# Kernel tuning notes

Hardware: AMD Instinct MI355X
Metric: run time of the kernel (lower is better)

Reference implementation:

```python
import jax, jax.numpy as jnp
import numpy as np

D = 1024      # n_embd
NH = 16       # attention heads
E = 8         # n_experts
K = 2         # k_best
FF = 4 * D    # expert MLP hidden
EPS = 1e-6    # rms_norm_epsilon
TEMP = 1.0    # target_temperature


def setup_inputs() -> dict:
    key = jax.random.key(0)
    ks = jax.random.split(key, 12)
    B, S = 2, 1024
    s = 0.02
    return {
        "x": jax.random.normal(ks[0], (B, S, D), jnp.float32),
        "attn_norm_w": jnp.ones((D,), jnp.float32),
        "wq": jax.random.normal(ks[1], (D, D), jnp.float32) * s,
        "wk": jax.random.normal(ks[2], (D, D), jnp.float32) * s,
        "wv": jax.random.normal(ks[3], (D, D), jnp.float32) * s,
        "wo": jax.random.normal(ks[4], (D, D), jnp.float32) * s,
        "mlp_norm_w": jnp.ones((D,), jnp.float32),
        "router_w": jax.random.normal(ks[5], (D, E), jnp.float32) * s,
        "w1": jax.random.normal(ks[6], (E, D, FF), jnp.float32) * s,
        "b1": jnp.zeros((E, FF), jnp.float32),
        "w2": jax.random.normal(ks[7], (E, FF, D), jnp.float32) * s,
        "b2": jnp.zeros((E, D), jnp.float32),
    }


def _rmsnorm(x, w):
    var = jnp.mean(jnp.square(x), axis=-1, keepdims=True)
    return x * jax.lax.rsqrt(var + EPS) * w


def _attention(x, wq, wk, wv, wo):
    B, S, _ = x.shape
    dh = D // NH
    q = (x @ wq).reshape(B, S, NH, dh)
    k = (x @ wk).reshape(B, S, NH, dh)
    v = (x @ wv).reshape(B, S, NH, dh)
    scores = jnp.einsum("bqhd,bkhd->bhqk", q, k) / jnp.sqrt(jnp.float32(dh))
    causal = jnp.tril(jnp.ones((S, S), bool))  # [S,S]
    scores = jnp.where(causal[None, None], scores, jnp.finfo(scores.dtype).min)
    attn = jax.nn.softmax(scores, axis=-1)
    out = jnp.einsum("bhqk,bkhd->bqhd", attn, v).reshape(B, S, D)
    return out @ wo


def reference(x, attn_norm_w, wq, wk, wv, wo, mlp_norm_w, router_w, w1, b1, w2, b2):
    B, S, _ = x.shape
    # attention sub-block
    x = x + _attention(_rmsnorm(x, attn_norm_w), wq, wk, wv, wo)
    residual = x
    h = _rmsnorm(x, mlp_norm_w)  # [B,S,D]

    # router: temperature softmax + top-k
    logits = h @ router_w / TEMP                      # [B,S,E]
    probs = jax.nn.softmax(logits, axis=-1)
    top_k_scores, top_k_indices = jax.lax.top_k(probs, K)  # [B,S,K]
    onehot = jax.nn.one_hot(top_k_indices, E, dtype=h.dtype)  # [B,S,K,E]
    gates = jnp.einsum("bsk,bske->bse", top_k_scores, onehot)  # [B,S,E]

    # load-balancing loss (Switch-style) + expert counts
    counts = jnp.sum(onehot, axis=(0, 1, 2))          # [E]
    frac = counts / (B * S * K)
    mean_prob = jnp.mean(probs, axis=(0, 1))          # [E]
    balancing_loss = E * jnp.sum(frac * mean_prob)

    # experts: dense dispatch; tokens with zero gate contribute nothing,
    # so this matches the sort/gather/scatter top-k combine exactly.
    pre = jnp.einsum("bsd,edf->ebsf", h, w1) + b1[:, None, None]  # [E,B,S,FF]
    act = jax.nn.gelu(pre)
    y = jnp.einsum("ebsf,efd->ebsd", act, w2) + b2[:, None, None]  # [E,B,S,D]
    moe = jnp.einsum("ebsd,bse->bsd", y, gates)

    out = residual + moe
    return out, balancing_loss, counts
```

## Files before the change

### kernel.cpp

```cpp
#include <hip/hip_runtime.h>

typedef __bf16 bf16;
typedef __bf16 bf16x4 __attribute__((ext_vector_type(4)));
typedef __bf16 bf16x8 __attribute__((ext_vector_type(8)));
typedef float f32x4 __attribute__((ext_vector_type(4)));

#define D_   1024
#define S_   1024
#define B_   2
#define NTOK 2048
#define FF_  4096
#define NE   8
#define CAP  5120
#define OUTN 2097152

__device__ __forceinline__ float gelu_f(float x) {
    float u = 0.7978845608028654f * (x + 0.044715f * x * x * x);
    float a = fabsf(u);
    float e = __expf(-2.0f * a);
    float t = (1.0f - e) / (1.0f + e);
    t = copysignf(t, u);
    return 0.5f * x * (1.0f + t);
}

__device__ __forceinline__ void gload16(const void* g, void* l) {
    __builtin_amdgcn_global_load_lds((const __attribute__((address_space(1))) unsigned int*)g,
                                     (__attribute__((address_space(3))) unsigned int*)l,
                                     16, 0, 0);
}

#define VMCNT(n) asm volatile("s_waitcnt vmcnt(" n ")" ::: "memory")
#define BARRIER() do { asm volatile("" ::: "memory"); \
                       __builtin_amdgcn_s_barrier();  \
                       asm volatile("" ::: "memory"); } while (0)

__global__ __launch_bounds__(256) void rmsnorm_k(const float* __restrict__ x,
                                                 const float* __restrict__ w,
                                                 float* __restrict__ yf,
                                                 bf16* __restrict__ yhi,
                                                 bf16* __restrict__ ylo) {
    int row = blockIdx.x;
    int t = threadIdx.x;
    const float* xr = x + (size_t)row * D_;
    float4 v = *(const float4*)(xr + t * 4);
    float ss = v.x * v.x + v.y * v.y + v.z * v.z + v.w * v.w;
    for (int off = 32; off; off >>= 1) ss += __shfl_down(ss, off);
    __shared__ float wsum[4];
    if ((t & 63) == 0) wsum[t >> 6] = ss;
    __syncthreads();
    float tot = wsum[0] + wsum[1] + wsum[2] + wsum[3];
    float rr = rsqrtf(tot * (1.0f / D_) + 1e-6f);
    float4 wv = *(const float4*)(w + t * 4);
    float y[4];
    y[0] = v.x * rr * wv.x; y[1] = v.y * rr * wv.y;
    y[2] = v.z * rr * wv.z; y[3] = v.w * rr * wv.w;
    if (yf) *(float4*)(yf + (size_t)row * D_ + t * 4) = *(float4*)y;
    if (yhi) {
#pragma unroll
        for (int i = 0; i < 4; i++) {
            bf16 hi = (bf16)y[i];
            yhi[(size_t)row * D_ + t * 4 + i] = hi;
            if (ylo) ylo[(size_t)row * D_ + t * 4 + i] = (bf16)(y[i] - (float)hi);
        }
    }
}

__global__ __launch_bounds__(256) void trans_split_k(
    const float* __restrict__ w0, const float* __restrict__ w1p,
    const float* __restrict__ w2p, const float* __restrict__ w3,
    bf16* o0h, bf16* o0l, bf16* o1h, bf16* o1l,
    bf16* o2h, bf16* o2l, bf16* o3h, bf16* o3l) {
    int z = blockIdx.z;
    const float* src = (z == 0) ? w0 : (z == 1) ? w1p : (z == 2) ? w2p : w3;
    bf16* dh = (z == 0) ? o0h : (z == 1) ? o1h : (z == 2) ? o2h : o3h;
    bf16* dl = (z == 0) ? o0l : (z == 1) ? o1l : (z == 2) ? o2l : o3l;
    __shared__ float tl[32][33];
    int c0 = blockIdx.x * 32, r0 = blockIdx.y * 32;
    int tx = threadIdx.x & 31, ty = threadIdx.x >> 5;
#pragma unroll
    for (int i = 0; i < 4; i++) {
        int r = ty + i * 8;
        tl[r][tx] = src[(size_t)(r0 + r) * 1024 + c0 + tx];
    }
    __syncthreads();
#pragma unroll
    for (int i = 0; i < 4; i++) {
        int c = ty + i * 8;
        float v = tl[tx][c];
        bf16 hi = (bf16)v;
        dh[(size_t)(c0 + c) * 1024 + r0 + tx] = hi;
        dl[(size_t)(c0 + c) * 1024 + r0 + tx] = (bf16)(v - (float)hi);
    }
}

__global__ __launch_bounds__(256) void transpose_cast4_k(const float* __restrict__ in,
                                                         bf16* __restrict__ out,
                                                         int R, int C) {
    __shared__ float tl[64][65];
    size_t base = (size_t)blockIdx.z * R * C;
    const float* src = in + base;
    bf16* dst = out + base;
    int c0 = blockIdx.x * 64, r0 = blockIdx.y * 64;
    int t = threadIdx.x;
    int lr = t >> 4;
    int lc = (t & 15) * 4;
#pragma unroll
    for (int i = 0; i < 4; i++) {
        int r = lr + i * 16;
        float4 v = *(const float4*)(src + (size_t)(r0 + r) * C + c0 + lc);
        tl[r][lc] = v.x; tl[r][lc + 1] = v.y; tl[r][lc + 2] = v.z; tl[r][lc + 3] = v.w;
    }
    __syncthreads();
    int wc = t >> 4;
    int wr = (t & 15) * 4;
#pragma unroll
    for (int i = 0; i < 4; i++) {
        int c = wc + i * 16;
        bf16x4 o;
        o[0] = (bf16)tl[wr][c];     o[1] = (bf16)tl[wr + 1][c];
        o[2] = (bf16)tl[wr + 2][c]; o[3] = (bf16)tl[wr + 3][c];
        *(bf16x4*)(dst + (size_t)(c0 + c) * R + r0 + wr) = o;
    }
}

#define SPLIT_STAGE(bi, k0)                             \
    gload16(gah0 + (k0), Lah[bi] + wv * 512);           \
    gload16(gah1 + (k0), Lah[bi] + 2048 + wv * 512);    \
    gload16(gal0 + (k0), Lal[bi] + wv * 512);           \
    gload16(gal1 + (k0), Lal[bi] + 2048 + wv * 512);    \
    gload16(gbh0 + (k0), Lbh[bi] + wv * 512);           \
    gload16(gbh1 + (k0), Lbh[bi] + 2048 + wv * 512);    \
    gload16(gbl0 + (k0), Lbl[bi] + wv * 512);           \
    gload16(gbl1 + (k0), Lbl[bi] + 2048 + wv * 512);

#define SPLIT_COMPUTE(bi) {                                                            \
    bf16x8 fah[4], fal[4], fbh[4], fbl[4];                                             \
    _Pragma("unroll") for (int i = 0; i < 4; i++) {                                    \
        fah[i] = *(const bf16x8*)(Lah[bi] + ra_off[i]);                                \
        fal[i] = *(const bf16x8*)(Lal[bi] + ra_off[i]);                                \
        fbh[i] = *(const bf16x8*)(Lbh[bi] + rb_off[i]);                                \
        fbl[i] = *(const bf16x8*)(Lbl[bi] + rb_off[i]);                                \
    }                                                                                  \
    _Pragma("unroll") for (int mt = 0; mt < 4; mt++)                                   \
    _Pragma("unroll") for (int nt = 0; nt < 4; nt++) {                                 \
        acc[mt][nt] = __builtin_amdgcn_mfma_f32_16x16x32_bf16(fah[mt], fbh[nt], acc[mt][nt], 0, 0, 0); \
        acc[mt][nt] = __builtin_amdgcn_mfma_f32_16x16x32_bf16(fah[mt], fbl[nt], acc[mt][nt], 0, 0, 0); \
        acc[mt][nt] = __builtin_amdgcn_mfma_f32_16x16x32_bf16(fal[mt], fbh[nt], acc[mt][nt], 0, 0, 0); \
    } }

#define GEMM128_SPLIT_BODY(EPILOGUE)                                                   \
    __shared__ __align__(16) bf16 Lah[2][4096];                                        \
    __shared__ __align__(16) bf16 Lal[2][4096];                                        \
    __shared__ __align__(16) bf16 Lbh[2][4096];                                        \
    __shared__ __align__(16) bf16 Lbl[2][4096];                                        \
    int t = threadIdx.x;                                                               \
    int wv = t >> 6, ln = t & 63;                                                      \
    int wm = wv >> 1, wn = wv & 1, l15 = ln & 15, qd = ln >> 4;                        \
    int sr0 = t >> 2, sr1 = 64 + sr0, cl = t & 3;                                      \
    int cs0 = (cl ^ ((sr0 >> 1) & 3)) * 8;                                             \
    int cs1 = (cl ^ ((sr1 >> 1) & 3)) * 8;                                             \
    const bf16* gah0 = Ah + (size_t)(m0 + sr0) * 1024 + cs0;                           \
    const bf16* gah1 = Ah + (size_t)(m0 + sr1) * 1024 + cs1;                           \
    const bf16* gal0 = Al + (size_t)(m0 + sr0) * 1024 + cs0;                           \
    const bf16* gal1 = Al + (size_t)(m0 + sr1) * 1024 + cs1;                           \
    const bf16* gbh0 = Bh + (size_t)(n0 + sr0) * 1024 + cs0;                           \
    const bf16* gbh1 = Bh + (size_t)(n0 + sr1) * 1024 + cs1;                           \
    const bf16* gbl0 = Bl + (size_t)(n0 + sr0) * 1024 + cs0;                           \
    const bf16* gbl1 = Bl + (size_t)(n0 + sr1) * 1024 + cs1;                           \
    int ra_off[4], rb_off[4];                                                          \
    _Pragma("unroll") for (int i = 0; i < 4; i++) {                                    \
        int r1 = wm * 64 + i * 16 + l15;                                               \
        ra_off[i] = r1 * 32 + (qd ^ ((r1 >> 1) & 3)) * 8;                              \
        int r2 = wn * 64 + i * 16 + l15;                                               \
        rb_off[i] = r2 * 32 + (qd ^ ((r2 >> 1) & 3)) * 8;                              \
    }                                                                                  \
    f32x4 acc[4][4];                                                                   \
    _Pragma("unroll") for (int mt = 0; mt < 4; mt++)                                   \
    _Pragma("unroll") for (int nt = 0; nt < 4; nt++) acc[mt][nt] = (f32x4){0.f,0.f,0.f,0.f}; \
    SPLIT_STAGE(0, 0);                                                                 \
    __syncthreads();                                                                   \
    for (int k0 = 0; k0 < 1024; k0 += 64) {                                            \
        SPLIT_STAGE(1, k0 + 32);                                                       \
        SPLIT_COMPUTE(0);                                                              \
        __syncthreads();                                                               \
        if (k0 + 64 < 1024) { SPLIT_STAGE(0, k0 + 64); }                               \
        SPLIT_COMPUTE(1);                                                              \
        __syncthreads();                                                               \
    }                                                                                  \
    _Pragma("unroll") for (int mt = 0; mt < 4; mt++)                                   \
    _Pragma("unroll") for (int nt = 0; nt < 4; nt++)                                   \
        _Pragma("unroll") for (int r = 0; r < 4; r++) {                                \
            int gm = m0 + wm * 64 + mt * 16 + qd * 4 + r;                              \
            int gn = n0 + wn * 64 + nt * 16 + l15;                                     \
            float vv = acc[mt][nt][r];                                                 \
            EPILOGUE                                                                   \
        }

__global__ __launch_bounds__(256) void gemm_qkv_k(
    const bf16* __restrict__ Ah, const bf16* __restrict__ Al,
    const bf16* __restrict__ Bqh, const bf16* __restrict__ Bql,
    const bf16* __restrict__ Bkh, const bf16* __restrict__ Bkl,
    const bf16* __restrict__ Bvh, const bf16* __restrict__ Bvl,
    bf16* Cqh, bf16* Cql, bf16* Ckh, bf16* Ckl, bf16* Cvh, bf16* Cvl) {
    int gy = blockIdx.y, zw = gy >> 3;
    const bf16* Bh = (zw == 0) ? Bqh : (zw == 1) ? Bkh : Bvh;
    const bf16* Bl = (zw == 0) ? Bql : (zw == 1) ? Bkl : Bvl;
    bf16* Ch = (zw == 0) ? Cqh : (zw == 1) ? Ckh : Cvh;
    bf16* Cl = (zw == 0) ? Cql : (zw == 1) ? Ckl : Cvl;
    int m0 = blockIdx.x * 128, n0 = (gy & 7) * 128;
    GEMM128_SPLIT_BODY({
        bf16 hi = (bf16)vv;
        Ch[(size_t)gm * D_ + gn] = hi;
        Cl[(size_t)gm * D_ + gn] = (bf16)(vv - (float)hi);
    })
}

__global__ __launch_bounds__(256) void gemm_wo_k(
    const bf16* __restrict__ Ah, const bf16* __restrict__ Al,
    const bf16* __restrict__ Bh, const bf16* __restrict__ Bl,
    float* __restrict__ C, const float* __restrict__ X) {
    int m0 = blockIdx.x * 128, n0 = blockIdx.y * 128;
    GEMM128_SPLIT_BODY({
        C[(size_t)gm * D_ + gn] = X[(size_t)gm * D_ + gn] + vv;
    })
}

#define AP 72

__global__ __launch_bounds__(256) void attn_mfma_k(
    const bf16* __restrict__ qhp, const bf16* __restrict__ qlp,
    const bf16* __restrict__ khp, const bf16* __restrict__ klp,
    const bf16* __restrict__ vhp, const bf16* __restrict__ vlp,
    bf16* __restrict__ aoh, bf16* __restrict__ aol) {
    int qt = (int)gridDim.x - 1 - (int)blockIdx.x;
    int h = blockIdx.y, b = blockIdx.z;
    __shared__ bf16 Ksh[64 * AP], Ksl[64 * AP], VTh[64 * AP], VTl[64 * AP];
    __shared__ bf16 Ph[4][16 * AP], Pl[4][16 * AP];
    int t = threadIdx.x, wv = t >> 6, ln = t & 63, l15 = ln & 15, qd = ln >> 4;

    bf16x8 aqh[2], aql[2];
    {
        size_t qb = ((size_t)(b * S_ + qt * 64 + wv * 16 + l15)) * D_ + h * 64 + qd * 8;
        aqh[0] = *(const bf16x8*)(qhp + qb);
        aqh[1] = *(const bf16x8*)(qhp + qb + 32);
        aql[0] = *(const bf16x8*)(qlp + qb);
        aql[1] = *(const bf16x8*)(qlp + qb + 32);
    }
    f32x4 oacc[4];
    float mrow[4], lrow[4];
#pragma unroll
    for (int i = 0; i < 4; i++) {
        oacc[i] = (f32x4){0.f, 0.f, 0.f, 0.f};
        mrow[i] = -1e30f; lrow[i] = 0.0f;
    }

    for (int kt = 0; kt <= qt; kt++) {
        __syncthreads();
#pragma unroll
        for (int j = 0; j < 2; j++) {
            int idx = t + j * 256;
            int row = idx >> 3, ch = (idx & 7) * 8;
            size_t g = ((size_t)(b * S_ + kt * 64 + row)) * D_ + h * 64 + ch;
            *(bf16x8*)&Ksh[row * AP + ch] = *(const bf16x8*)(khp + g);
            *(bf16x8*)&Ksl[row * AP + ch] = *(const bf16x8*)(klp + g);
            bf16x8 vvh = *(const bf16x8*)(vhp + g);
            bf16x8 vvl = *(const bf16x8*)(vlp + g);
#pragma unroll
            for (int jj = 0; jj < 8; jj++) {
                VTh[(ch + jj) * AP + row] = vvh[jj];
                VTl[(ch + jj) * AP + row] = vvl[jj];
            }
        }
        __syncthreads();

        f32x4 sacc[4];
#pragma unroll
        for (int nt = 0; nt < 4; nt++) sacc[nt] = (f32x4){0.f, 0.f, 0.f, 0.f};
#pragma unroll
        for (int ks = 0; ks < 2; ks++) {
#pragma unroll
            for (int nt = 0; nt < 4; nt++) {
                bf16x8 bh = *(const bf16x8*)&Ksh[(nt * 16 + l15) * AP + ks * 32 + qd * 8];
                bf16x8 bl = *(const bf16x8*)&Ksl[(nt * 16 + l15) * AP + ks * 32 + qd * 8];
                sacc[nt] = __builtin_amdgcn_mfma_f32_16x16x32_bf16(aqh[ks], bh, sacc[nt], 0, 0, 0);
                sacc[nt] = __builtin_amdgcn_mfma_f32_16x16x32_bf16(aqh[ks], bl, sacc[nt], 0, 0, 0);
                sacc[nt] = __builtin_amdgcn_mfma_f32_16x16x32_bf16(aql[ks], bh, sacc[nt], 0, 0, 0);
            }
        }
        bool diag = (kt == qt);
#pragma unroll
        for (int r = 0; r < 4; r++) {
            float s0[4];
#pragma unroll
            for (int nt = 0; nt < 4; nt++) {
                s0[nt] = sacc[nt][r] * 0.125f;
                if (diag && (nt * 16 + l15) > (wv * 16 + qd * 4 + r)) s0[nt] = -1e30f;
            }
            float vmax = fmaxf(fmaxf(s0[0], s0[1]), fmaxf(s0[2], s0[3]));
            for (int off = 1; off < 16; off <<= 1) vmax = fmaxf(vmax, __shfl_xor(vmax, off));
            float mnew = fmaxf(mrow[r], vmax);
            float alpha = __expf(mrow[r] - mnew);
            float p[4], rs = 0.0f;
#pragma unroll
            for (int nt = 0; nt < 4; nt++) { p[nt] = __expf(s0[nt] - mnew); rs += p[nt]; }
            for (int off = 1; off < 16; off <<= 1) rs += __shfl_xor(rs, off);
            lrow[r] = lrow[r] * alpha + rs;
            mrow[r] = mnew;
#pragma unroll
            for (int nt = 0; nt < 4; nt++) oacc[nt][r] *= alpha;
            int prow = qd * 4 + r;
#pragma unroll
            for (int nt = 0; nt < 4; nt++) {
                bf16 hi = (bf16)p[nt];
                Ph[wv][prow * AP + nt * 16 + l15] = hi;
                Pl[wv][prow * AP + nt * 16 + l15] = (bf16)(p[nt] - (float)hi);
            }
        }
#pragma unroll
        for (int ks2 = 0; ks2 < 2; ks2++) {
            bf16x8 aph = *(const bf16x8*)&Ph[wv][l15 * AP + ks2 * 32 + qd * 8];
            bf16x8 apl = *(const bf16x8*)&Pl[wv][l15 * AP + ks2 * 32 + qd * 8];
#pragma unroll
            for (int nt = 0; nt < 4; nt++) {
                bf16x8 bvh = *(const bf16x8*)&VTh[(nt * 16 + l15) * AP + ks2 * 32 + qd * 8];
                bf16x8 bvl = *(const bf16x8*)&VTl[(nt * 16 + l15) * AP + ks2 * 32 + qd * 8];
                oacc[nt] = __builtin_amdgcn_mfma_f32_16x16x32_bf16(aph, bvh, oacc[nt], 0, 0, 0);
                oacc[nt] = __builtin_amdgcn_mfma_f32_16x16x32_bf16(aph, bvl, oacc[nt], 0, 0, 0);
                oacc[nt] = __builtin_amdgcn_mfma_f32_16x16x32_bf16(apl, bvh, oacc[nt], 0, 0, 0);
            }
        }
    }

#pragma unroll
    for (int r = 0; r < 4; r++) {
        float inv = 1.0f / lrow[r];
        size_t rowa = ((size_t)(b * S_ + qt * 64 + wv * 16 + qd * 4 + r)) * D_ + h * 64;
#pragma unroll
        for (int nt = 0; nt < 4; nt++) {
            float o = oacc[nt][r] * inv;
            bf16 hi = (bf16)o;
            aoh[rowa + nt * 16 + l15] = hi;
            aol[rowa + nt * 16 + l15] = (bf16)(o - (float)hi);
        }
    }
}

__global__ __launch_bounds__(256) void router_k(const float* __restrict__ h,
                                                const float* __restrict__ rw,
                                                int* __restrict__ tidx,
                                                float* __restrict__ tgate,
                                                int* __restrict__ ecnt,
                                                float* __restrict__ psum) {
    int wv = threadIdx.x >> 6, ln = threadIdx.x & 63;
    int tok = blockIdx.x * 4 + wv;
    const float* hr = h + (size_t)tok * D_;
    float acc[NE];
#pragma unroll
    for (int e = 0; e < NE; e++) acc[e] = 0.0f;
    int base = ln * 16;
#pragma unroll
    for (int c = 0; c < 4; c++) {
        float4 hv = *(const float4*)(hr + base + c * 4);
        const float* rp = rw + (size_t)(base + c * 4) * NE;
        float hx[4] = {hv.x, hv.y, hv.z, hv.w};
#pragma unroll
        for (int jj = 0; jj < 4; jj++)
#pragma unroll
            for (int e = 0; e < NE; e++)
                acc[e] = fmaf(hx[jj], rp[jj * NE + e], acc[e]);
    }
#pragma unroll
    for (int e = 0; e < NE; e++)
        for (int off = 32; off; off >>= 1) acc[e] += __shfl_down(acc[e], off);

    __shared__ float pb[4][NE];
    if (ln == 0) {
        float mx = acc[0];
#pragma unroll
        for (int e = 1; e < NE; e++) mx = fmaxf(mx, acc[e]);
        float p[NE], ssum = 0.0f;
#pragma unroll
        for (int e = 0; e < NE; e++) { p[e] = expf(acc[e] - mx); ssum += p[e]; }
        float inv = 1.0f / ssum;
#pragma unroll
        for (int e = 0; e < NE; e++) p[e] *= inv;
        int i0 = 0; float b0 = p[0];
#pragma unroll
        for (int e = 1; e < NE; e++) if (p[e] > b0) { b0 = p[e]; i0 = e; }
        int i1 = -1; float b1v = -1.0f;
#pragma unroll
        for (int e = 0; e < NE; e++) if (e != i0 && p[e] > b1v) { b1v = p[e]; i1 = e; }
        tidx[tok * 2] = i0; tidx[tok * 2 + 1] = i1;
        tgate[tok * 2] = b0; tgate[tok * 2 + 1] = b1v;
        atomicAdd(&ecnt[i0], 1);
        atomicAdd(&ecnt[i1], 1);
#pragma unroll
        for (int e = 0; e < NE; e++) pb[wv][e] = p[e];
    }
    __syncthreads();
    if (threadIdx.x < NE) {
        float s2 = pb[0][threadIdx.x] + pb[1][threadIdx.x] + pb[2][threadIdx.x] + pb[3][threadIdx.x];
        atomicAdd(&psum[threadIdx.x], s2);
    }
}

__global__ void passb_k(const int* __restrict__ ecnt, const float* __restrict__ psum,
                        int* __restrict__ eoffp, int* __restrict__ ecnt2,
                        float* __restrict__ out_tail) {
    if (threadIdx.x == 0) {
        int off = 0; float loss = 0.0f;
        for (int e = 0; e < NE; e++) {
            eoffp[e] = off;
            int c = ecnt[e];
            off += (c + 127) & ~127;
            loss += (c * (1.0f / 4096.0f)) * (psum[e] * (1.0f / 2048.0f));
            out_tail[1 + e] = (float)c;
            ecnt2[e] = 0;
        }
        eoffp[NE] = off;
        out_tail[0] = 8.0f * loss;
    }
}

__global__ __launch_bounds__(256) void scatter_k(const int* __restrict__ tidx,
                                                 const int* __restrict__ eoffp,
                                                 int* __restrict__ ecnt2,
                                                 int* __restrict__ stok,
                                                 int* __restrict__ sidx) {
    int tok = blockIdx.x * 256 + threadIdx.x;
    for (int k = 0; k < 2; k++) {
        int e = tidx[tok * 2 + k];
        int pos = eoffp[e] + atomicAdd(&ecnt2[e], 1);
        stok[pos] = tok;
        sidx[tok * 2 + k] = pos;
    }
}

#define MOE_STAGE(bufA, bufB, k0)                       \
    gload16(ga0 + (k0), (bufA) + wv * 512);             \
    gload16(ga1 + (k0), (bufA) + 2048 + wv * 512);      \
    gload16(gb0 + (k0), (bufB) + wv * 512);             \
    gload16(gb1 + (k0), (bufB) + 2048 + wv * 512);

#define MOE_TILE(bufA, bufB) {                                                         \
    bf16x8 af[4], bfr[4];                                                              \
    _Pragma("unroll") for (int i = 0; i < 4; i++) {                                    \
        af[i]  = *(const bf16x8*)((bufA) + ra_off[i]);                                 \
        bfr[i] = *(const bf16x8*)((bufB) + rb_off[i]);                                 \
    }                                                                                  \
    _Pragma("unroll") for (int mt = 0; mt < 4; mt++)                                   \
    _Pragma("unroll") for (int nt = 0; nt < 4; nt++)                                   \
        acc[mt][nt] = __builtin_amdgcn_mfma_f32_16x16x32_bf16(af[mt], bfr[nt], acc[mt][nt], 0, 0, 0); }

#define MOE_STEP(rdA, rdB, VM)      \
    VMCNT(VM);                      \
    BARRIER();                      \
    MOE_TILE(rdA, rdB);             \
    BARRIER();

__global__ __launch_bounds__(256) void moe_gemm1_k(const bf16* __restrict__ hB,
                                                   const bf16* __restrict__ w1t,
                                                   const float* __restrict__ b1,
                                                   const int* __restrict__ eoffp,
                                                   const int* __restrict__ stok,
                                                   bf16* __restrict__ act) {
    int m0 = blockIdx.x * 128, n0 = blockIdx.y * 128;
    if (m0 >= eoffp[NE]) return;
    int e = 0;
#pragma unroll
    for (int i = 1; i < NE; i++) if (m0 >= eoffp[i]) e = i;

    __shared__ __align__(16) bf16 As[2][4096];
    __shared__ __align__(16) bf16 Bs[2][4096];
    int t = threadIdx.x;
    int wv = t >> 6, ln = t & 63;
    int wm = wv >> 1, wn = wv & 1, l15 = ln & 15, qd = ln >> 4;

    int sr0 = t >> 2, sr1 = 64 + sr0, cl = t & 3;
    int cs0 = (cl ^ ((sr0 >> 1) & 3)) * 8;
    int cs1 = (cl ^ ((sr1 >> 1) & 3)) * 8;
    const bf16* ga0 = hB + (size_t)stok[m0 + sr0] * D_ + cs0;
    const bf16* ga1 = hB + (size_t)stok[m0 + sr1] * D_ + cs1;
    const bf16* Bb = w1t + ((size_t)e * FF_ + n0) * D_;
    const bf16* gb0 = Bb + (size_t)sr0 * D_ + cs0;
    const bf16* gb1 = Bb + (size_t)sr1 * D_ + cs1;

    int ra_off[4], rb_off[4];
#pragma unroll
    for (int i = 0; i < 4; i++) {
        int r1 = wm * 64 + i * 16 + l15;
        ra_off[i] = r1 * 32 + (qd ^ ((r1 >> 1) & 3)) * 8;
        int r2 = wn * 64 + i * 16 + l15;
        rb_off[i] = r2 * 32 + (qd ^ ((r2 >> 1) & 3)) * 8;
    }

    f32x4 acc[4][4];
#pragma unroll
    for (int mt = 0; mt < 4; mt++)
#pragma unroll
        for (int nt = 0; nt < 4; nt++) acc[mt][nt] = (f32x4){0.f, 0.f, 0.f, 0.f};

    MOE_STAGE(As[0], Bs[0], 0);
    for (int k0 = 0; k0 < 960; k0 += 64) {
        MOE_STAGE(As[1], Bs[1], k0 + 32);
        MOE_STEP(As[0], Bs[0], "4");
        MOE_STAGE(As[0], Bs[0], k0 + 64);
        MOE_STEP(As[1], Bs[1], "4");
    }
    MOE_STAGE(As[1], Bs[1], 992);
    MOE_STEP(As[0], Bs[0], "4");
    MOE_STEP(As[1], Bs[1], "0");

    const float* b1e = b1 + (size_t)e * FF_;
#pragma unroll
    for (int mt = 0; mt < 4; mt++)
#pragma unroll
        for (int nt = 0; nt < 4; nt++) {
            int gn = n0 + wn * 64 + nt * 16 + l15;
            float bias = b1e[gn];
#pragma unroll
            for (int r = 0; r < 4; r++) {
                int gm = m0 + wm * 64 + mt * 16 + qd * 4 + r;
                act[(size_t)gm * FF_ + gn] = (bf16)gelu_f(acc[mt][nt][r] + bias);
            }
        }
}

__global__ __launch_bounds__(256) void moe_gemm2_k(const bf16* __restrict__ act,
                                                   const bf16* __restrict__ w2t,
                                                   const float* __restrict__ b2,
                                                   const int* __restrict__ eoffp,
                                                   float* __restrict__ y) {
    int m0 = blockIdx.x * 128, n0 = blockIdx.y * 128;
    if (m0 >= eoffp[NE]) return;
    int e = 0;
#pragma unroll
    for (int i = 1; i < NE; i++) if (m0 >= eoffp[i]) e = i;
    int zk = blockIdx.z;
    int kbase = zk * 2048;

    __shared__ __align__(16) bf16 As[4][4096];
    __shared__ __align__(16) bf16 Bs[4][4096];
    int t = threadIdx.x;
    int wv = t >> 6, ln = t & 63;
    int wm = wv >> 1, wn = wv & 1, l15 = ln & 15, qd = ln >> 4;

    int sr0 = t >> 2, sr1 = 64 + sr0, cl = t & 3;
    int cs0 = (cl ^ ((sr0 >> 1) & 3)) * 8;
    int cs1 = (cl ^ ((sr1 >> 1) & 3)) * 8;
    const bf16* ga0 = act + (size_t)(m0 + sr0) * FF_ + kbase + cs0;
    const bf16* ga1 = act + (size_t)(m0 + sr1) * FF_ + kbase + cs1;
    const bf16* Bb = w2t + ((size_t)e * D_ + n0) * FF_;
    const bf16* gb0 = Bb + (size_t)sr0 * FF_ + kbase + cs0;
    const bf16* gb1 = Bb + (size_t)sr1 * FF_ + kbase + cs1;

    int ra_off[4], rb_off[4];
#pragma unroll
    for (int i = 0; i < 4; i++) {
        int r1 = wm * 64 + i * 16 + l15;
        ra_off[i] = r1 * 32 + (qd ^ ((r1 >> 1) & 3)) * 8;
        int r2 = wn * 64 + i * 16 + l15;
        rb_off[i] = r2 * 32 + (qd ^ ((r2 >> 1) & 3)) * 8;
    }

    f32x4 acc[4][4];
#pragma unroll
    for (int mt = 0; mt < 4; mt++)
#pragma unroll
        for (int nt = 0; nt < 4; nt++) acc[mt][nt] = (f32x4){0.f, 0.f, 0.f, 0.f};

    MOE_STAGE(As[0], Bs[0], 0);
    MOE_STAGE(As[1], Bs[1], 32);
    for (int k0 = 0; k0 < 1920; k0 += 128) {
        MOE_STAGE(As[2], Bs[2], k0 + 64);  MOE_STEP(As[0], Bs[0], "8");
        MOE_STAGE(As[3], Bs[3], k0 + 96);  MOE_STEP(As[1], Bs[1], "8");
        MOE_STAGE(As[0], Bs[0], k0 + 128); MOE_STEP(As[2], Bs[2], "8");
        MOE_STAGE(As[1], Bs[1], k0 + 160); MOE_STEP(As[3], Bs[3], "8");
    }
    MOE_STAGE(As[2], Bs[2], 1984); MOE_STEP(As[0], Bs[0], "8");
    MOE_STAGE(As[3], Bs[3], 2016); MOE_STEP(As[1], Bs[1], "8");
    MOE_STEP(As[2], Bs[2], "4");
    MOE_STEP(As[3], Bs[3], "0");

    const float* b2e = b2 + (size_t)e * D_;
#pragma unroll
    for (int mt = 0; mt < 4; mt++)
#pragma unroll
        for (int nt = 0; nt < 4; nt++) {
            int gn = n0 + wn * 64 + nt * 16 + l15;
            float bias = (zk == 0) ? b2e[gn] : 0.0f;
#pragma unroll
            for (int r = 0; r < 4; r++) {
                int gm = m0 + wm * 64 + mt * 16 + qd * 4 + r;
                atomicAdd(&y[(size_t)gm * D_ + gn], acc[mt][nt][r] + bias);
            }
        }
}

__global__ __launch_bounds__(256) void combine_k(const float* __restrict__ y,
                                                 const int* __restrict__ sidx,
                                                 const float* __restrict__ tgate,
                                                 float* __restrict__ out) {
    int tok = blockIdx.x;
    int d = threadIdx.x * 4;
    int s0 = sidx[tok * 2], s1 = sidx[tok * 2 + 1];
    float g0 = tgate[tok * 2], g1 = tgate[tok * 2 + 1];
    float4 a = *(const float4*)(y + (size_t)s0 * D_ + d);
    float4 b = *(const float4*)(y + (size_t)s1 * D_ + d);
    float4 o = *(const float4*)(out + (size_t)tok * D_ + d);
    o.x += g0 * a.x + g1 * b.x;
    o.y += g0 * a.y + g1 * b.y;
    o.z += g0 * a.z + g1 * b.z;
    o.w += g0 * a.w + g1 * b.w;
    *(float4*)(out + (size_t)tok * D_ + d) = o;
}

extern "C" void kernel_launch(void* const* d_in, const int* in_sizes, int n_in,
                              void* d_out, int out_size, void* d_ws, size_t ws_size,
                              hipStream_t stream) {
    const float* x   = (const float*)d_in[0];
    const float* anw = (const float*)d_in[1];
    const float* wq  = (const float*)d_in[2];
    const float* wk  = (const float*)d_in[3];
    const float* wv  = (const float*)d_in[4];
    const float* wo  = (const float*)d_in[5];
    const float* mnw = (const float*)d_in[6];
    const float* rw  = (const float*)d_in[7];
    const float* w1  = (const float*)d_in[8];
    const float* b1  = (const float*)d_in[9];
    const float* w2  = (const float*)d_in[10];
    const float* b2  = (const float*)d_in[11];
    float* out = (float*)d_out;

    char* p = (char*)d_ws;
    auto take = [&](size_t n) { char* r = p; p += (n + 255) & ~(size_t)255; return r; };
    bf16* h1h = (bf16*)take((size_t)OUTN * 2);
    bf16* h1l = (bf16*)take((size_t)OUTN * 2);
    bf16* qh  = (bf16*)take((size_t)OUTN * 2);
    bf16* ql  = (bf16*)take((size_t)OUTN * 2);
    bf16* kh  = (bf16*)take((size_t)OUTN * 2);
    bf16* kl  = (bf16*)take((size_t)OUTN * 2);
    bf16* vh  = (bf16*)take((size_t)OUTN * 2);
    bf16* vl  = (bf16*)take((size_t)OUTN * 2);
    bf16* wqth = (bf16*)take((size_t)D_ * D_ * 2);
    bf16* wqtl = (bf16*)take((size_t)D_ * D_ * 2);
    bf16* wkth = (bf16*)take((size_t)D_ * D_ * 2);
    bf16* wktl = (bf16*)take((size_t)D_ * D_ * 2);
    bf16* wvth = (bf16*)take((size_t)D_ * D_ * 2);
    bf16* wvtl = (bf16*)take((size_t)D_ * D_ * 2);
    bf16* woth = (bf16*)take((size_t)D_ * D_ * 2);
    bf16* wotl = (bf16*)take((size_t)D_ * D_ * 2);
    bf16* w1t = (bf16*)take((size_t)NE * FF_ * D_ * 2);
    bf16* w2t = (bf16*)take((size_t)NE * FF_ * D_ * 2);
    bf16* act = (bf16*)take((size_t)CAP * FF_ * 2);
    int*   tidx  = (int*)take(NTOK * 2 * 4);
    float* tgate = (float*)take(NTOK * 2 * 4);
    int*   sidx  = (int*)take(NTOK * 2 * 4);
    int*   ecnt  = (int*)take(64);
    int*   ecnt2 = (int*)take(64);
    float* psum  = (float*)take(64);
    int*   eoffp = (int*)take(64);
    int*   stok  = (int*)take(CAP * 4);

    bf16*  aoh = h1h;
    bf16*  aol = h1l;
    float* h_f = (float*)qh;
    bf16*  h_b = kh;
    float* y   = (float*)vh;

    hipMemsetAsync(ecnt, 0, NE * 4, stream);
    hipMemsetAsync(psum, 0, NE * 4, stream);
    hipMemsetAsync(stok, 0, CAP * 4, stream);

    trans_split_k<<<dim3(32, 32, 4), 256, 0, stream>>>(wq, wk, wv, wo,
        wqth, wqtl, wkth, wktl, wvth, wvtl, woth, wotl);
    transpose_cast4_k<<<dim3(FF_ / 64, D_ / 64, NE), 256, 0, stream>>>(w1, w1t, D_, FF_);
    transpose_cast4_k<<<dim3(D_ / 64, FF_ / 64, NE), 256, 0, stream>>>(w2, w2t, FF_, D_);

    rmsnorm_k<<<NTOK, 256, 0, stream>>>(x, anw, nullptr, h1h, h1l);
    gemm_qkv_k<<<dim3(16, 24), 256, 0, stream>>>(h1h, h1l,
        wqth, wqtl, wkth, wktl, wvth, wvtl, qh, ql, kh, kl, vh, vl);
    attn_mfma_k<<<dim3(16, 16, 2), 256, 0, stream>>>(qh, ql, kh, kl, vh, vl, aoh, aol);
    gemm_wo_k<<<dim3(16, 8), 256, 0, stream>>>(aoh, aol, woth, wotl, out, x);

    hipMemsetAsync(y, 0, (size_t)CAP * D_ * 4, stream);
    rmsnorm_k<<<NTOK, 256, 0, stream>>>(out, mnw, h_f, h_b, nullptr);
    router_k<<<NTOK / 4, 256, 0, stream>>>(h_f, rw, tidx, tgate, ecnt, psum);
    passb_k<<<1, 64, 0, stream>>>(ecnt, psum, eoffp, ecnt2, out + OUTN);
    scatter_k<<<NTOK / 256, 256, 0, stream>>>(tidx, eoffp, ecnt2, stok, sidx);
    moe_gemm1_k<<<dim3(CAP / 128, FF_ / 128), 256, 0, stream>>>(h_b, w1t, b1, eoffp, stok, act);
    moe_gemm2_k<<<dim3(CAP / 128, D_ / 128, 2), 256, 0, stream>>>(act, w2t, b2, eoffp, y);
    combine_k<<<NTOK, 256, 0, stream>>>(y, sidx, tgate, out);
}
```

Measured before the change: 795.7 us.

## Split-K the Wo GEMM with atomics, un-split MoE GEMM2, pipeline split GEMMs

The Wo projection now runs as a 4-way split-K with atomic adds into an output that is pre-filled with x by a device copy, which gives 512 blocks instead of 128. The second MoE GEMM drops its 2-way split-K and writes results directly, so the memset of y and the atomics go away. The QKV/Wo GEMMs switch to vmcnt-based waits with explicit barriers for finer load/compute overlap. The Wo split adds atomic traffic and an extra 8MB copy, while the un-split MoE GEMM2 has fewer blocks and a longer K loop.

Measured after the change: 776.1 us. -2.5%, faster.

```diff
diff --git a/kernel.cpp b/kernel.cpp
--- a/kernel.cpp
+++ b/kernel.cpp
@@ -148,7 +148,13 @@
         acc[mt][nt] = __builtin_amdgcn_mfma_f32_16x16x32_bf16(fal[mt], fbh[nt], acc[mt][nt], 0, 0, 0); \
     } }
 
-#define GEMM128_SPLIT_BODY(EPILOGUE)                                                   \
+#define SPLIT_STEP(bi, VM)          \
+    VMCNT(VM);                      \
+    BARRIER();                      \
+    SPLIT_COMPUTE(bi);              \
+    BARRIER();
+
+#define SPLIT_DECLS(KOFF)                                                              \
     __shared__ __align__(16) bf16 Lah[2][4096];                                        \
     __shared__ __align__(16) bf16 Lal[2][4096];                                        \
     __shared__ __align__(16) bf16 Lbh[2][4096];                                        \
@@ -159,14 +165,14 @@
     int sr0 = t >> 2, sr1 = 64 + sr0, cl = t & 3;                                      \
     int cs0 = (cl ^ ((sr0 >> 1) & 3)) * 8;                                             \
     int cs1 = (cl ^ ((sr1 >> 1) & 3)) * 8;                                             \
-    const bf16* gah0 = Ah + (size_t)(m0 + sr0) * 1024 + cs0;                           \
-    const bf16* gah1 = Ah + (size_t)(m0 + sr1) * 1024 + cs1;                           \
-    const bf16* gal0 = Al + (size_t)(m0 + sr0) * 1024 + cs0;                           \
-    const bf16* gal1 = Al + (size_t)(m0 + sr1) * 1024 + cs1;                           \
-    const bf16* gbh0 = Bh + (size_t)(n0 + sr0) * 1024 + cs0;                           \
-    const bf16* gbh1 = Bh + (size_t)(n0 + sr1) * 1024 + cs1;                           \
-    const bf16* gbl0 = Bl + (size_t)(n0 + sr0) * 1024 + cs0;                           \
-    const bf16* gbl1 = Bl + (size_t)(n0 + sr1) * 1024 + cs1;                           \
+    const bf16* gah0 = Ah + (size_t)(m0 + sr0) * 1024 + (KOFF) + cs0;                  \
+    const bf16* gah1 = Ah + (size_t)(m0 + sr1) * 1024 + (KOFF) + cs1;                  \
+    const bf16* gal0 = Al + (size_t)(m0 + sr0) * 1024 + (KOFF) + cs0;                  \
+    const bf16* gal1 = Al + (size_t)(m0 + sr1) * 1024 + (KOFF) + cs1;                  \
+    const bf16* gbh0 = Bh + (size_t)(n0 + sr0) * 1024 + (KOFF) + cs0;                  \
+    const bf16* gbh1 = Bh + (size_t)(n0 + sr1) * 1024 + (KOFF) + cs1;                  \
+    const bf16* gbl0 = Bl + (size_t)(n0 + sr0) * 1024 + (KOFF) + cs0;                  \
+    const bf16* gbl1 = Bl + (size_t)(n0 + sr1) * 1024 + (KOFF) + cs1;                  \
     int ra_off[4], rb_off[4];                                                          \
     _Pragma("unroll") for (int i = 0; i < 4; i++) {                                    \
         int r1 = wm * 64 + i * 16 + l15;                                               \
@@ -176,25 +182,7 @@
     }                                                                                  \
     f32x4 acc[4][4];                                                                   \
     _Pragma("unroll") for (int mt = 0; mt < 4; mt++)                                   \
-    _Pragma("unroll") for (int nt = 0; nt < 4; nt++) acc[mt][nt] = (f32x4){0.f,0.f,0.f,0.f}; \
-    SPLIT_STAGE(0, 0);                                                                 \
-    __syncthreads();                                                                   \
-    for (int k0 = 0; k0 < 1024; k0 += 64) {                                            \
-        SPLIT_STAGE(1, k0 + 32);                                                       \
-        SPLIT_COMPUTE(0);                                                              \
-        __syncthreads();                                                               \
-        if (k0 + 64 < 1024) { SPLIT_STAGE(0, k0 + 64); }                               \
-        SPLIT_COMPUTE(1);                                                              \
-        __syncthreads();                                                               \
-    }                                                                                  \
-    _Pragma("unroll") for (int mt = 0; mt < 4; mt++)                                   \
-    _Pragma("unroll") for (int nt = 0; nt < 4; nt++)                                   \
-        _Pragma("unroll") for (int r = 0; r < 4; r++) {                                \
-            int gm = m0 + wm * 64 + mt * 16 + qd * 4 + r;                              \
-            int gn = n0 + wn * 64 + nt * 16 + l15;                                     \
-            float vv = acc[mt][nt][r];                                                 \
-            EPILOGUE                                                                   \
-        }
+    _Pragma("unroll") for (int nt = 0; nt < 4; nt++) acc[mt][nt] = (f32x4){0.f,0.f,0.f,0.f};
 
 __global__ __launch_bounds__(256) void gemm_qkv_k(
     const bf16* __restrict__ Ah, const bf16* __restrict__ Al,
@@ -208,21 +196,59 @@
     bf16* Ch = (zw == 0) ? Cqh : (zw == 1) ? Ckh : Cvh;
     bf16* Cl = (zw == 0) ? Cql : (zw == 1) ? Ckl : Cvl;
     int m0 = blockIdx.x * 128, n0 = (gy & 7) * 128;
-    GEMM128_SPLIT_BODY({
-        bf16 hi = (bf16)vv;
-        Ch[(size_t)gm * D_ + gn] = hi;
-        Cl[(size_t)gm * D_ + gn] = (bf16)(vv - (float)hi);
-    })
+    SPLIT_DECLS(0)
+    SPLIT_STAGE(0, 0);
+    for (int k0 = 0; k0 < 960; k0 += 64) {
+        SPLIT_STAGE(1, k0 + 32);
+        SPLIT_STEP(0, "8");
+        SPLIT_STAGE(0, k0 + 64);
+        SPLIT_STEP(1, "8");
+    }
+    SPLIT_STAGE(1, 992);
+    SPLIT_STEP(0, "8");
+    SPLIT_STEP(1, "0");
+#pragma unroll
+    for (int mt = 0; mt < 4; mt++)
+#pragma unroll
+        for (int nt = 0; nt < 4; nt++)
+#pragma unroll
+            for (int r = 0; r < 4; r++) {
+                int gm = m0 + wm * 64 + mt * 16 + qd * 4 + r;
+                int gn = n0 + wn * 64 + nt * 16 + l15;
+                float vv = acc[mt][nt][r];
+                bf16 hi = (bf16)vv;
+                Ch[(size_t)gm * D_ + gn] = hi;
+                Cl[(size_t)gm * D_ + gn] = (bf16)(vv - (float)hi);
+            }
 }
 
 __global__ __launch_bounds__(256) void gemm_wo_k(
     const bf16* __restrict__ Ah, const bf16* __restrict__ Al,
     const bf16* __restrict__ Bh, const bf16* __restrict__ Bl,
-    float* __restrict__ C, const float* __restrict__ X) {
+    float* __restrict__ C) {
     int m0 = blockIdx.x * 128, n0 = blockIdx.y * 128;
-    GEMM128_SPLIT_BODY({
-        C[(size_t)gm * D_ + gn] = X[(size_t)gm * D_ + gn] + vv;
-    })
+    int kb = blockIdx.z * 256;
+    SPLIT_DECLS(kb)
+    SPLIT_STAGE(0, 0);
+    for (int k0 = 0; k0 < 192; k0 += 64) {
+        SPLIT_STAGE(1, k0 + 32);
+        SPLIT_STEP(0, "8");
+        SPLIT_STAGE(0, k0 + 64);
+        SPLIT_STEP(1, "8");
+    }
+    SPLIT_STAGE(1, 224);
+    SPLIT_STEP(0, "8");
+    SPLIT_STEP(1, "0");
+#pragma unroll
+    for (int mt = 0; mt < 4; mt++)
+#pragma unroll
+        for (int nt = 0; nt < 4; nt++)
+#pragma unroll
+            for (int r = 0; r < 4; r++) {
+                int gm = m0 + wm * 64 + mt * 16 + qd * 4 + r;
+                int gn = n0 + wn * 64 + nt * 16 + l15;
+                atomicAdd(&C[(size_t)gm * D_ + gn], acc[mt][nt][r]);
+            }
 }
 
 #define AP 72
@@ -536,8 +562,6 @@
     int e = 0;
 #pragma unroll
     for (int i = 1; i < NE; i++) if (m0 >= eoffp[i]) e = i;
-    int zk = blockIdx.z;
-    int kbase = zk * 2048;
 
     __shared__ __align__(16) bf16 As[4][4096];
     __shared__ __align__(16) bf16 Bs[4][4096];
@@ -548,11 +572,11 @@
     int sr0 = t >> 2, sr1 = 64 + sr0, cl = t & 3;
     int cs0 = (cl ^ ((sr0 >> 1) & 3)) * 8;
     int cs1 = (cl ^ ((sr1 >> 1) & 3)) * 8;
-    const bf16* ga0 = act + (size_t)(m0 + sr0) * FF_ + kbase + cs0;
-    const bf16* ga1 = act + (size_t)(m0 + sr1) * FF_ + kbase + cs1;
+    const bf16* ga0 = act + (size_t)(m0 + sr0) * FF_ + cs0;
+    const bf16* ga1 = act + (size_t)(m0 + sr1) * FF_ + cs1;
     const bf16* Bb = w2t + ((size_t)e * D_ + n0) * FF_;
-    const bf16* gb0 = Bb + (size_t)sr0 * FF_ + kbase + cs0;
-    const bf16* gb1 = Bb + (size_t)sr1 * FF_ + kbase + cs1;
+    const bf16* gb0 = Bb + (size_t)sr0 * FF_ + cs0;
+    const bf16* gb1 = Bb + (size_t)sr1 * FF_ + cs1;
 
     int ra_off[4], rb_off[4];
 #pragma unroll
@@ -571,14 +595,14 @@
 
     MOE_STAGE(As[0], Bs[0], 0);
     MOE_STAGE(As[1], Bs[1], 32);
-    for (int k0 = 0; k0 < 1920; k0 += 128) {
+    for (int k0 = 0; k0 < 3968; k0 += 128) {
         MOE_STAGE(As[2], Bs[2], k0 + 64);  MOE_STEP(As[0], Bs[0], "8");
         MOE_STAGE(As[3], Bs[3], k0 + 96);  MOE_STEP(As[1], Bs[1], "8");
         MOE_STAGE(As[0], Bs[0], k0 + 128); MOE_STEP(As[2], Bs[2], "8");
         MOE_STAGE(As[1], Bs[1], k0 + 160); MOE_STEP(As[3], Bs[3], "8");
     }
-    MOE_STAGE(As[2], Bs[2], 1984); MOE_STEP(As[0], Bs[0], "8");
-    MOE_STAGE(As[3], Bs[3], 2016); MOE_STEP(As[1], Bs[1], "8");
+    MOE_STAGE(As[2], Bs[2], 4032); MOE_STEP(As[0], Bs[0], "8");
+    MOE_STAGE(As[3], Bs[3], 4064); MOE_STEP(As[1], Bs[1], "8");
     MOE_STEP(As[2], Bs[2], "4");
     MOE_STEP(As[3], Bs[3], "0");
 
@@ -588,11 +612,11 @@
 #pragma unroll
         for (int nt = 0; nt < 4; nt++) {
             int gn = n0 + wn * 64 + nt * 16 + l15;
-            float bias = (zk == 0) ? b2e[gn] : 0.0f;
+            float bias = b2e[gn];
 #pragma unroll
             for (int r = 0; r < 4; r++) {
                 int gm = m0 + wm * 64 + mt * 16 + qd * 4 + r;
-                atomicAdd(&y[(size_t)gm * D_ + gn], acc[mt][nt][r] + bias);
+                y[(size_t)gm * D_ + gn] = acc[mt][nt][r] + bias;
             }
         }
 }
@@ -671,6 +695,7 @@
     hipMemsetAsync(ecnt, 0, NE * 4, stream);
     hipMemsetAsync(psum, 0, NE * 4, stream);
     hipMemsetAsync(stok, 0, CAP * 4, stream);
+    hipMemcpyAsync(out, x, (size_t)OUTN * 4, hipMemcpyDeviceToDevice, stream);
 
     trans_split_k<<<dim3(32, 32, 4), 256, 0, stream>>>(wq, wk, wv, wo,
         wqth, wqtl, wkth, wktl, wvth, wvtl, woth, wotl);
@@ -681,14 +706,13 @@
     gemm_qkv_k<<<dim3(16, 24), 256, 0, stream>>>(h1h, h1l,
         wqth, wqtl, wkth, wktl, wvth, wvtl, qh, ql, kh, kl, vh, vl);
     attn_mfma_k<<<dim3(16, 16, 2), 256, 0, stream>>>(qh, ql, kh, kl, vh, vl, aoh, aol);
-    gemm_wo_k<<<dim3(16, 8), 256, 0, stream>>>(aoh, aol, woth, wotl, out, x);
-
-    hipMemsetAsync(y, 0, (size_t)CAP * D_ * 4, stream);
+    gemm_wo_k<<<dim3(16, 8, 4), 256, 0, stream>>>(aoh, aol, woth, wotl, out);
+
     rmsnorm_k<<<NTOK, 256, 0, stream>>>(out, mnw, h_f, h_b, nullptr);
     router_k<<<NTOK / 4, 256, 0, stream>>>(h_f, rw, tidx, tgate, ecnt, psum);
     passb_k<<<1, 64, 0, stream>>>(ecnt, psum, eoffp, ecnt2, out + OUTN);
     scatter_k<<<NTOK / 256, 256, 0, stream>>>(tidx, eoffp, ecnt2, stok, sidx);
     moe_gemm1_k<<<dim3(CAP / 128, FF_ / 128), 256, 0, stream>>>(h_b, w1t, b1, eoffp, stok, act);
-    moe_gemm2_k<<<dim3(CAP / 128, D_ / 128, 2), 256, 0, stream>>>(act, w2t, b2, eoffp, y);
+    moe_gemm2_k<<<dim3(CAP / 128, D_ / 128), 256, 0, stream>>>(act, w2t, b2, eoffp, y);
     combine_k<<<NTOK, 256, 0, stream>>>(y, sidx, tgate, out);
 }
```
